# Kernel optimization log

Measured on AMD Instinct MI355X. Metric: run time of the kernel, lower is better.

The kernel has to match this reference:

```python
import jax, jax.numpy as jnp
import numpy as np

N_NODES = 250_000
N_EDGES = 4_000_000


def setup_inputs() -> dict:
    key = jax.random.key(0)
    ks = jax.random.split(key, 8)
    x = jax.random.normal(ks[0], (N_NODES, 3), dtype=jnp.float32)
    w = jax.random.normal(ks[1], (N_EDGES, 4), dtype=jnp.float32)
    # MLP params: Linear(10->40), ReLU, Linear(40->4); torch Linear layout [out, in]
    W1 = jax.random.normal(ks[2], (40, 10), dtype=jnp.float32) * (1.0 / np.sqrt(10.0))
    b1 = jax.random.normal(ks[3], (40,), dtype=jnp.float32) * 0.01
    W2 = jax.random.normal(ks[4], (4, 40), dtype=jnp.float32) * (1.0 / np.sqrt(40.0))
    b2 = jax.random.normal(ks[5], (4,), dtype=jnp.float32) * 0.01
    src = jax.random.randint(ks[6], (N_EDGES,), 0, N_NODES, dtype=jnp.int64)
    dst = jax.random.randint(ks[7], (N_EDGES,), 0, N_NODES, dtype=jnp.int64)
    return {"x": x, "w": w, "W1": W1, "b1": b1, "W2": W2, "b2": b2,
            "src": src, "dst": dst}


def reference(x, w, W1, b1, W2, b2, src, dst):
    x_src = x[src]                                  # [E, 3] gather
    x_dst = x[dst]                                  # [E, 3] gather
    m = jnp.concatenate([x_src, x_dst, w], axis=1)  # [E, 10]
    h = jax.nn.relu(m @ W1.T + b1)                  # [E, 40]
    w_out = h @ W2.T + b2                           # [E, 4]
    e_tilde = jnp.concatenate([x_src, w_out], axis=1)  # [E, 7]
    return w_out, e_tilde
```

## Files before the change

kernel.cpp:

```cpp
#include <hip/hip_runtime.h>

typedef __fp16 h2 __attribute__((ext_vector_type(2)));
typedef float f4 __attribute__((ext_vector_type(4)));

static __device__ __forceinline__ unsigned pkrtz(float a, float b) {
    union { h2 v; unsigned u; } cv;
    cv.v = __builtin_amdgcn_cvt_pkrtz(a, b);
    return cv.u;
}
static __device__ __forceinline__ h2 as_h2(unsigned u) {
    union { unsigned u; h2 v; } cv; cv.u = u; return cv.v;
}

__global__ void prep_kernel(const float* __restrict__ W1, const float* __restrict__ b1,
                            const float* __restrict__ W2, const float* __restrict__ b2,
                            unsigned* __restrict__ ws) {
    const int t = threadIdx.x;
    if (t < 40) {
        #pragma unroll
        for (int i = 0; i < 5; ++i)
            ws[t * 6 + i] = pkrtz(W1[t * 10 + 2 * i], W1[t * 10 + 2 * i + 1]);
        ws[t * 6 + 5] = __float_as_uint(b1[t]);
    } else if (t < 60) {
        const int p = t - 40;
        #pragma unroll
        for (int o = 0; o < 4; ++o)
            ws[240 + p * 4 + o] = pkrtz(W2[o * 40 + 2 * p], W2[o * 40 + 2 * p + 1]);
    } else if (t < 64) {
        ws[320 + (t - 60)] = __float_as_uint(b2[t - 60]);
    }
}

#define TPB 256

__global__ __launch_bounds__(TPB) void edge_mlp_nt2_kernel(
    const float* __restrict__ x,
    const float* __restrict__ w,
    const int* __restrict__ src,
    const int* __restrict__ dst,
    const unsigned* __restrict__ W,
    float* __restrict__ w_out,
    float* __restrict__ e_tilde,
    int E)
{
    __shared__ float s_et[4][64 * 7];

    const int t    = threadIdx.x;
    const int wave = t >> 6;
    const int lane = t & 63;
    const int e    = blockIdx.x * TPB + t;

    float m0 = 0.f, m1 = 0.f, m2 = 0.f;
    h2 vm0 = as_h2(0), vm1 = as_h2(0), vm2 = as_h2(0), vm3 = as_h2(0), vm4 = as_h2(0);

    if (e < E) {
        const int si = __builtin_nontemporal_load(src + e);
        const int di = __builtin_nontemporal_load(dst + e);
        m0 = x[3 * si]; m1 = x[3 * si + 1]; m2 = x[3 * si + 2];
        const float d0 = x[3 * di], d1 = x[3 * di + 1], d2 = x[3 * di + 2];
        const f4 wv = __builtin_nontemporal_load((const f4*)w + e);
        vm0 = as_h2(pkrtz(m0, m1));
        vm1 = as_h2(pkrtz(m2, d0));
        vm2 = as_h2(pkrtz(d1, d2));
        vm3 = as_h2(pkrtz(wv.x, wv.y));
        vm4 = as_h2(pkrtz(wv.z, wv.w));
    }

    float o0 = __uint_as_float(W[320]);
    float o1 = __uint_as_float(W[321]);
    float o2 = __uint_as_float(W[322]);
    float o3 = __uint_as_float(W[323]);

    #pragma unroll
    for (int jp = 0; jp < 20; ++jp) {
        const int j0 = 2 * jp, j1 = 2 * jp + 1;
        float h0v = __uint_as_float(W[j0 * 6 + 5]);
        float h1v = __uint_as_float(W[j1 * 6 + 5]);
        h0v = __builtin_amdgcn_fdot2(vm0, as_h2(W[j0 * 6 + 0]), h0v, false);
        h1v = __builtin_amdgcn_fdot2(vm0, as_h2(W[j1 * 6 + 0]), h1v, false);
        h0v = __builtin_amdgcn_fdot2(vm1, as_h2(W[j0 * 6 + 1]), h0v, false);
        h1v = __builtin_amdgcn_fdot2(vm1, as_h2(W[j1 * 6 + 1]), h1v, false);
        h0v = __builtin_amdgcn_fdot2(vm2, as_h2(W[j0 * 6 + 2]), h0v, false);
        h1v = __builtin_amdgcn_fdot2(vm2, as_h2(W[j1 * 6 + 2]), h1v, false);
        h0v = __builtin_amdgcn_fdot2(vm3, as_h2(W[j0 * 6 + 3]), h0v, false);
        h1v = __builtin_amdgcn_fdot2(vm3, as_h2(W[j1 * 6 + 3]), h1v, false);
        h0v = __builtin_amdgcn_fdot2(vm4, as_h2(W[j0 * 6 + 4]), h0v, false);
        h1v = __builtin_amdgcn_fdot2(vm4, as_h2(W[j1 * 6 + 4]), h1v, false);
        h0v = fmaxf(h0v, 0.f);
        h1v = fmaxf(h1v, 0.f);
        const h2 hp = as_h2(pkrtz(h0v, h1v));
        o0 = __builtin_amdgcn_fdot2(hp, as_h2(W[240 + jp * 4 + 0]), o0, false);
        o1 = __builtin_amdgcn_fdot2(hp, as_h2(W[240 + jp * 4 + 1]), o1, false);
        o2 = __builtin_amdgcn_fdot2(hp, as_h2(W[240 + jp * 4 + 2]), o2, false);
        o3 = __builtin_amdgcn_fdot2(hp, as_h2(W[240 + jp * 4 + 3]), o3, false);
    }

    if (e < E) {
        f4 ov; ov.x = o0; ov.y = o1; ov.z = o2; ov.w = o3;
        __builtin_nontemporal_store(ov, (f4*)w_out + e);
    }

    float* sw = s_et[wave];
    sw[lane * 7 + 0] = m0;
    sw[lane * 7 + 1] = m1;
    sw[lane * 7 + 2] = m2;
    sw[lane * 7 + 3] = o0;
    sw[lane * 7 + 4] = o1;
    sw[lane * 7 + 5] = o2;
    sw[lane * 7 + 6] = o3;

    const int base_e = blockIdx.x * TPB + wave * 64;
    const long long fbase = (long long)base_e * 7;
    if (base_e + 64 <= E) {
        f4* dst4 = (f4*)(e_tilde + fbase);
        {
            f4 v0; v0.x = sw[4 * lane]; v0.y = sw[4 * lane + 1];
            v0.z = sw[4 * lane + 2]; v0.w = sw[4 * lane + 3];
            __builtin_nontemporal_store(v0, dst4 + lane);
        }
        if (lane < 48) {
            const int i2 = 64 + lane;
            f4 v1; v1.x = sw[4 * i2]; v1.y = sw[4 * i2 + 1];
            v1.z = sw[4 * i2 + 2]; v1.w = sw[4 * i2 + 3];
            __builtin_nontemporal_store(v1, dst4 + i2);
        }
    } else {
        const int nvalid = (E - base_e < 64 ? (E - base_e) : 64) * 7;
        #pragma unroll
        for (int k = 0; k < 7; ++k) {
            const int idx = lane + 64 * k;
            if (idx < nvalid)
                __builtin_nontemporal_store(sw[idx], e_tilde + fbase + idx);
        }
    }
}

extern "C" void kernel_launch(void* const* d_in, const int* in_sizes, int n_in,
                              void* d_out, int out_size, void* d_ws, size_t ws_size,
                              hipStream_t stream) {
    const float* x  = (const float*)d_in[0];
    const float* w  = (const float*)d_in[1];
    const float* W1 = (const float*)d_in[2];
    const float* b1 = (const float*)d_in[3];
    const float* W2 = (const float*)d_in[4];
    const float* b2 = (const float*)d_in[5];
    const int* src  = (const int*)d_in[6];
    const int* dst  = (const int*)d_in[7];

    const int E = in_sizes[6];

    float* w_out   = (float*)d_out;
    float* e_tilde = w_out + (size_t)E * 4;
    unsigned* ws   = (unsigned*)d_ws;

    prep_kernel<<<1, 64, 0, stream>>>(W1, b1, W2, b2, ws);

    const int nblocks = (E + TPB - 1) / TPB;
    edge_mlp_nt2_kernel<<<nblocks, TPB, 0, stream>>>(
        x, w, src, dst, ws, w_out, e_tilde, E);
}
```

Measured before the change: 101.2 us.

## Convert edge MLP to grid-stride persistent kernel with software-pipelined gathers

The kernel now launches at most 2048 blocks and loops grid-stride over edges. It software-pipelines the loads: the indices for iteration i+2 and the x gathers and w loads for iteration i+1 are issued while iteration i runs its MLP and stores. The aim is to hide the latency of the random gathers behind compute without relying only on occupancy. In exchange the kernel holds more registers for prefetched values, which could lower occupancy, and it has fewer waves in flight to hide latency.

Result: slower. 121.2 us (+19.7%).

```diff
diff --git a/kernel.cpp b/kernel.cpp
--- a/kernel.cpp
+++ b/kernel.cpp
@@ -33,7 +33,7 @@
 
 #define TPB 256
 
-__global__ __launch_bounds__(TPB) void edge_mlp_nt2_kernel(
+__global__ __launch_bounds__(TPB) void edge_mlp_pipe_kernel(
     const float* __restrict__ x,
     const float* __restrict__ w,
     const int* __restrict__ src,
@@ -41,97 +41,131 @@
     const unsigned* __restrict__ W,
     float* __restrict__ w_out,
     float* __restrict__ e_tilde,
-    int E)
+    int E, int S)
 {
     __shared__ float s_et[4][64 * 7];
 
     const int t    = threadIdx.x;
     const int wave = t >> 6;
     const int lane = t & 63;
-    const int e    = blockIdx.x * TPB + t;
 
-    float m0 = 0.f, m1 = 0.f, m2 = 0.f;
-    h2 vm0 = as_h2(0), vm1 = as_h2(0), vm2 = as_h2(0), vm3 = as_h2(0), vm4 = as_h2(0);
+    int eA = blockIdx.x * TPB + t;
+    int eB = eA + S;
+    int eC = eB + S;
 
-    if (e < E) {
-        const int si = __builtin_nontemporal_load(src + e);
-        const int di = __builtin_nontemporal_load(dst + e);
-        m0 = x[3 * si]; m1 = x[3 * si + 1]; m2 = x[3 * si + 2];
-        const float d0 = x[3 * di], d1 = x[3 * di + 1], d2 = x[3 * di + 2];
-        const f4 wv = __builtin_nontemporal_load((const f4*)w + e);
-        vm0 = as_h2(pkrtz(m0, m1));
-        vm1 = as_h2(pkrtz(m2, d0));
-        vm2 = as_h2(pkrtz(d1, d2));
-        vm3 = as_h2(pkrtz(wv.x, wv.y));
-        vm4 = as_h2(pkrtz(wv.z, wv.w));
+    int siB = 0, diB = 0;
+    float a0 = 0.f, a1 = 0.f, a2 = 0.f, a3 = 0.f, a4 = 0.f, a5 = 0.f;
+    f4 wvA = {0.f, 0.f, 0.f, 0.f};
+    {
+        int siA = 0, diA = 0;
+        if (eA < E) {
+            siA = __builtin_nontemporal_load(src + eA);
+            diA = __builtin_nontemporal_load(dst + eA);
+        }
+        if (eB < E) {
+            siB = __builtin_nontemporal_load(src + eB);
+            diB = __builtin_nontemporal_load(dst + eB);
+        }
+        if (eA < E) {
+            a0 = x[3 * siA]; a1 = x[3 * siA + 1]; a2 = x[3 * siA + 2];
+            a3 = x[3 * diA]; a4 = x[3 * diA + 1]; a5 = x[3 * diA + 2];
+            wvA = __builtin_nontemporal_load((const f4*)w + eA);
+        }
     }
 
-    float o0 = __uint_as_float(W[320]);
-    float o1 = __uint_as_float(W[321]);
-    float o2 = __uint_as_float(W[322]);
-    float o3 = __uint_as_float(W[323]);
+    for (int base = blockIdx.x * TPB; base < E; base += S) {
+        float b0 = 0.f, b1v = 0.f, b2v = 0.f, b3 = 0.f, b4 = 0.f, b5 = 0.f;
+        f4 wvB = {0.f, 0.f, 0.f, 0.f};
+        if (eB < E) {
+            b0 = x[3 * siB]; b1v = x[3 * siB + 1]; b2v = x[3 * siB + 2];
+            b3 = x[3 * diB]; b4 = x[3 * diB + 1]; b5 = x[3 * diB + 2];
+            wvB = __builtin_nontemporal_load((const f4*)w + eB);
+        }
+        int siC = 0, diC = 0;
+        if (eC < E) {
+            siC = __builtin_nontemporal_load(src + eC);
+            diC = __builtin_nontemporal_load(dst + eC);
+        }
 
-    #pragma unroll
-    for (int jp = 0; jp < 20; ++jp) {
-        const int j0 = 2 * jp, j1 = 2 * jp + 1;
-        float h0v = __uint_as_float(W[j0 * 6 + 5]);
-        float h1v = __uint_as_float(W[j1 * 6 + 5]);
-        h0v = __builtin_amdgcn_fdot2(vm0, as_h2(W[j0 * 6 + 0]), h0v, false);
-        h1v = __builtin_amdgcn_fdot2(vm0, as_h2(W[j1 * 6 + 0]), h1v, false);
-        h0v = __builtin_amdgcn_fdot2(vm1, as_h2(W[j0 * 6 + 1]), h0v, false);
-        h1v = __builtin_amdgcn_fdot2(vm1, as_h2(W[j1 * 6 + 1]), h1v, false);
-        h0v = __builtin_amdgcn_fdot2(vm2, as_h2(W[j0 * 6 + 2]), h0v, false);
-        h1v = __builtin_amdgcn_fdot2(vm2, as_h2(W[j1 * 6 + 2]), h1v, false);
-        h0v = __builtin_amdgcn_fdot2(vm3, as_h2(W[j0 * 6 + 3]), h0v, false);
-        h1v = __builtin_amdgcn_fdot2(vm3, as_h2(W[j1 * 6 + 3]), h1v, false);
-        h0v = __builtin_amdgcn_fdot2(vm4, as_h2(W[j0 * 6 + 4]), h0v, false);
-        h1v = __builtin_amdgcn_fdot2(vm4, as_h2(W[j1 * 6 + 4]), h1v, false);
-        h0v = fmaxf(h0v, 0.f);
-        h1v = fmaxf(h1v, 0.f);
-        const h2 hp = as_h2(pkrtz(h0v, h1v));
-        o0 = __builtin_amdgcn_fdot2(hp, as_h2(W[240 + jp * 4 + 0]), o0, false);
-        o1 = __builtin_amdgcn_fdot2(hp, as_h2(W[240 + jp * 4 + 1]), o1, false);
-        o2 = __builtin_amdgcn_fdot2(hp, as_h2(W[240 + jp * 4 + 2]), o2, false);
-        o3 = __builtin_amdgcn_fdot2(hp, as_h2(W[240 + jp * 4 + 3]), o3, false);
-    }
+        const h2 vm0 = as_h2(pkrtz(a0, a1));
+        const h2 vm1 = as_h2(pkrtz(a2, a3));
+        const h2 vm2 = as_h2(pkrtz(a4, a5));
+        const h2 vm3 = as_h2(pkrtz(wvA.x, wvA.y));
+        const h2 vm4 = as_h2(pkrtz(wvA.z, wvA.w));
 
-    if (e < E) {
-        f4 ov; ov.x = o0; ov.y = o1; ov.z = o2; ov.w = o3;
-        __builtin_nontemporal_store(ov, (f4*)w_out + e);
-    }
+        float o0 = __uint_as_float(W[320]);
+        float o1 = __uint_as_float(W[321]);
+        float o2 = __uint_as_float(W[322]);
+        float o3 = __uint_as_float(W[323]);
 
-    float* sw = s_et[wave];
-    sw[lane * 7 + 0] = m0;
-    sw[lane * 7 + 1] = m1;
-    sw[lane * 7 + 2] = m2;
-    sw[lane * 7 + 3] = o0;
-    sw[lane * 7 + 4] = o1;
-    sw[lane * 7 + 5] = o2;
-    sw[lane * 7 + 6] = o3;
+        #pragma unroll
+        for (int jp = 0; jp < 20; ++jp) {
+            const int j0 = 2 * jp, j1 = 2 * jp + 1;
+            float h0v = __uint_as_float(W[j0 * 6 + 5]);
+            float h1v = __uint_as_float(W[j1 * 6 + 5]);
+            h0v = __builtin_amdgcn_fdot2(vm0, as_h2(W[j0 * 6 + 0]), h0v, false);
+            h1v = __builtin_amdgcn_fdot2(vm0, as_h2(W[j1 * 6 + 0]), h1v, false);
+            h0v = __builtin_amdgcn_fdot2(vm1, as_h2(W[j0 * 6 + 1]), h0v, false);
+            h1v = __builtin_amdgcn_fdot2(vm1, as_h2(W[j1 * 6 + 1]), h1v, false);
+            h0v = __builtin_amdgcn_fdot2(vm2, as_h2(W[j0 * 6 + 2]), h0v, false);
+            h1v = __builtin_amdgcn_fdot2(vm2, as_h2(W[j1 * 6 + 2]), h1v, false);
+            h0v = __builtin_amdgcn_fdot2(vm3, as_h2(W[j0 * 6 + 3]), h0v, false);
+            h1v = __builtin_amdgcn_fdot2(vm3, as_h2(W[j1 * 6 + 3]), h1v, false);
+            h0v = __builtin_amdgcn_fdot2(vm4, as_h2(W[j0 * 6 + 4]), h0v, false);
+            h1v = __builtin_amdgcn_fdot2(vm4, as_h2(W[j1 * 6 + 4]), h1v, false);
+            h0v = fmaxf(h0v, 0.f);
+            h1v = fmaxf(h1v, 0.f);
+            const h2 hp = as_h2(pkrtz(h0v, h1v));
+            o0 = __builtin_amdgcn_fdot2(hp, as_h2(W[240 + jp * 4 + 0]), o0, false);
+            o1 = __builtin_amdgcn_fdot2(hp, as_h2(W[240 + jp * 4 + 1]), o1, false);
+            o2 = __builtin_amdgcn_fdot2(hp, as_h2(W[240 + jp * 4 + 2]), o2, false);
+            o3 = __builtin_amdgcn_fdot2(hp, as_h2(W[240 + jp * 4 + 3]), o3, false);
+        }
 
-    const int base_e = blockIdx.x * TPB + wave * 64;
-    const long long fbase = (long long)base_e * 7;
-    if (base_e + 64 <= E) {
-        f4* dst4 = (f4*)(e_tilde + fbase);
-        {
-            f4 v0; v0.x = sw[4 * lane]; v0.y = sw[4 * lane + 1];
-            v0.z = sw[4 * lane + 2]; v0.w = sw[4 * lane + 3];
-            __builtin_nontemporal_store(v0, dst4 + lane);
+        const int e = base + t;
+        if (e < E) {
+            f4 ov; ov.x = o0; ov.y = o1; ov.z = o2; ov.w = o3;
+            __builtin_nontemporal_store(ov, (f4*)w_out + e);
         }
-        if (lane < 48) {
-            const int i2 = 64 + lane;
-            f4 v1; v1.x = sw[4 * i2]; v1.y = sw[4 * i2 + 1];
-            v1.z = sw[4 * i2 + 2]; v1.w = sw[4 * i2 + 3];
-            __builtin_nontemporal_store(v1, dst4 + i2);
+
+        float* sw = s_et[wave];
+        sw[lane * 7 + 0] = a0;
+        sw[lane * 7 + 1] = a1;
+        sw[lane * 7 + 2] = a2;
+        sw[lane * 7 + 3] = o0;
+        sw[lane * 7 + 4] = o1;
+        sw[lane * 7 + 5] = o2;
+        sw[lane * 7 + 6] = o3;
+
+        const int base_e = base + wave * 64;
+        const long long fbase = (long long)base_e * 7;
+        if (base_e + 64 <= E) {
+            f4* dst4 = (f4*)(e_tilde + fbase);
+            {
+                f4 v0; v0.x = sw[4 * lane]; v0.y = sw[4 * lane + 1];
+                v0.z = sw[4 * lane + 2]; v0.w = sw[4 * lane + 3];
+                __builtin_nontemporal_store(v0, dst4 + lane);
+            }
+            if (lane < 48) {
+                const int i2 = 64 + lane;
+                f4 v1; v1.x = sw[4 * i2]; v1.y = sw[4 * i2 + 1];
+                v1.z = sw[4 * i2 + 2]; v1.w = sw[4 * i2 + 3];
+                __builtin_nontemporal_store(v1, dst4 + i2);
+            }
+        } else if (base_e < E) {
+            const int nvalid = (E - base_e) * 7;
+            #pragma unroll
+            for (int k = 0; k < 7; ++k) {
+                const int idx = lane + 64 * k;
+                if (idx < nvalid)
+                    __builtin_nontemporal_store(sw[idx], e_tilde + fbase + idx);
+            }
         }
-    } else {
-        const int nvalid = (E - base_e < 64 ? (E - base_e) : 64) * 7;
-        #pragma unroll
-        for (int k = 0; k < 7; ++k) {
-            const int idx = lane + 64 * k;
-            if (idx < nvalid)
-                __builtin_nontemporal_store(sw[idx], e_tilde + fbase + idx);
-        }
+
+        a0 = b0; a1 = b1v; a2 = b2v; a3 = b3; a4 = b4; a5 = b5;
+        wvA = wvB;
+        siB = siC; diB = diC;
+        eA = eB; eB = eC; eC += S;
     }
 }
 
@@ -155,7 +189,9 @@
 
     prep_kernel<<<1, 64, 0, stream>>>(W1, b1, W2, b2, ws);
 
-    const int nblocks = (E + TPB - 1) / TPB;
-    edge_mlp_nt2_kernel<<<nblocks, TPB, 0, stream>>>(
-        x, w, src, dst, ws, w_out, e_tilde, E);
+    int nblocks = (E + TPB - 1) / TPB;
+    if (nblocks > 2048) nblocks = 2048;
+    const int S = nblocks * TPB;
+    edge_mlp_pipe_kernel<<<nblocks, TPB, 0, stream>>>(
+        x, w, src, dst, ws, w_out, e_tilde, E, S);
 }
```
